# Kernel tuning notes

Hardware: AMD Instinct MI355X
Metric: run time of the kernel (lower is better)

Reference implementation:

```python
import jax, jax.numpy as jnp
import numpy as np

NUM_HEADS = 8
HEAD_DIM = 32  # in_channels // num_heads = 256 // 8


def setup_inputs() -> dict:
    key = jax.random.key(0)
    k1, k2, k3, k4 = jax.random.split(key, 4)
    B, C, H, W = 16, 256, 64, 64
    N = (H // 2) * (W // 2)  # 1024
    return {
        "x": jax.random.normal(k1, (B, C, H, W), dtype=jnp.float32),
        "w_qkv": jax.random.normal(k2, (3 * C, C), dtype=jnp.float32) * (1.0 / np.sqrt(C)),
        "b_qkv": jax.random.normal(k3, (3 * C,), dtype=jnp.float32) * 0.02,
        "pos_encoding": jax.random.normal(k4, (1, N, HEAD_DIM), dtype=jnp.float32) * 0.02,
    }


def reference(x, w_qkv, b_qkv, pos_encoding):
    B, C, H, W = x.shape
    Hp, Wp = H // 2, W // 2
    N = Hp * Wp
    # 1x1 conv: [B,C,H,W] -> [B,3C,H,W]
    y = jnp.einsum('bchw,oc->bohw', x, w_qkv) + b_qkv[None, :, None, None]
    # 2x2 max pool, stride 2
    y = y.reshape(B, 3 * C, Hp, 2, Wp, 2).max(axis=(3, 5))  # [B,3C,Hp,Wp]
    # split into q,k,v heads: channel order is (3, heads, head_dim)
    qkv = y.reshape(B, 3, NUM_HEADS, HEAD_DIM, N)
    qkv = qkv.transpose(1, 0, 2, 4, 3)  # [3,B,h,N,d]
    q, k, v = qkv[0], qkv[1], qkv[2]
    q = q + pos_encoding[:, None, :, :]  # broadcast over heads -> [B,h,N,d]
    scale = HEAD_DIM ** (-0.5)
    attn = jnp.einsum('bhnd,bhmd->bhnm', q, k) * scale
    attn = jax.nn.softmax(attn, axis=-1)
    out = jnp.einsum('bhnm,bhmd->bhnd', attn, v)  # [B,h,N,d]
    # transpose(2,3) then reshape -> [B, C, Hp, Wp]
    out = out.transpose(0, 1, 3, 2).reshape(B, C, Hp, Wp)
    return out
```

## Files before the change

### kernel.cpp

```cpp
#include <hip/hip_runtime.h>
#include <hip/hip_bf16.h>

typedef __bf16 bf16;
typedef bf16 bf16x8 __attribute__((ext_vector_type(8)));
typedef float f32x4 __attribute__((ext_vector_type(4)));
typedef float f32x16 __attribute__((ext_vector_type(16)));
typedef unsigned int u32;
typedef u32 u32x2 __attribute__((ext_vector_type(2)));
typedef u32 u32x4 __attribute__((ext_vector_type(4)));
typedef int i32x2 __attribute__((ext_vector_type(2)));


__device__ __forceinline__ u32 packbf2(float lo, float hi) {
    unsigned short a = __builtin_bit_cast(unsigned short, (bf16)lo);
    unsigned short b = __builtin_bit_cast(unsigned short, (bf16)hi);
    return (u32)a | ((u32)b << 16);
}

#if __has_builtin(__builtin_amdgcn_exp2f)
#define EXP2(x) __builtin_amdgcn_exp2f(x)
#else
#define EXP2(x) __expf((x)*0.69314718055994531f)
#endif

__device__ __forceinline__ i32x2 pl32swap(u32 a, u32 b) {
#if __has_builtin(__builtin_amdgcn_permlane32_swap)
    return __builtin_amdgcn_permlane32_swap((int)a, (int)b, false, false);
#else
    int lid = __builtin_amdgcn_mbcnt_hi(~0u, __builtin_amdgcn_mbcnt_lo(~0u, 0));
    u32 ax = (u32)__shfl_xor((int)a, 32);
    u32 bx = (u32)__shfl_xor((int)b, 32);
    i32x2 r;
    r.x = (int)(lid < 32 ? a : bx);
    r.y = (int)(lid < 32 ? ax : b);
    return r;
#endif
}

__device__ __forceinline__ f32x16 zero16() {
    f32x16 z;
#pragma unroll
    for (int i = 0; i < 16; ++i) z[i] = 0.f;
    return z;
}

__device__ __forceinline__ void gload_lds16(const bf16* gsrc, bf16* ldst) {
    __builtin_amdgcn_global_load_lds(
        (const __attribute__((address_space(1))) void*)gsrc,
        (__attribute__((address_space(3))) void*)ldst, 16, 0, 0);
}

#define MEMFENCE()                               \
    do {                                         \
        asm volatile("" ::: "memory");           \
        __builtin_amdgcn_sched_barrier(0);       \
    } while (0)

#define WAITV(N)                                                   \
    do {                                                           \
        asm volatile("s_waitcnt vmcnt(" #N ")" ::: "memory");      \
        __builtin_amdgcn_sched_barrier(0);                         \
    } while (0)

#define WAITLGKM()                                                 \
    do {                                                           \
        asm volatile("s_waitcnt lgkmcnt(0)" ::: "memory");         \
        __builtin_amdgcn_sched_barrier(0);                         \
    } while (0)

__global__ __launch_bounds__(256) void k_transpose_x(const float* __restrict__ x,
                                                     bf16* __restrict__ xt) {
    __shared__ __align__(16) bf16 tile[64][72];
    int b = blockIdx.z, cb = blockIdx.y, pb = blockIdx.x;
    int c0 = cb * 64, p0 = pb * 64;
    int t = threadIdx.x;
    int pr = (t & 15) * 4;
    int cr = t >> 4;
    const float* xp = x + ((size_t)(b * 256 + c0)) * 4096 + p0;
    for (int pass = 0; pass < 4; ++pass) {
        int c = cr + pass * 16;
        float4 v = *reinterpret_cast<const float4*>(xp + (size_t)c * 4096 + pr);
        tile[pr + 0][c] = (bf16)v.x;
        tile[pr + 1][c] = (bf16)v.y;
        tile[pr + 2][c] = (bf16)v.z;
        tile[pr + 3][c] = (bf16)v.w;
    }
    __syncthreads();
    bf16* op = xt + ((size_t)(b * 4096 + p0)) * 256 + c0;
    int c8 = (t & 7) * 8;
    int prow = t >> 3;
    for (int pass = 0; pass < 2; ++pass) {
        int p = prow + pass * 32;
        *reinterpret_cast<bf16x8*>(op + (size_t)p * 256 + c8) =
            *reinterpret_cast<const bf16x8*>(&tile[p][c8]);
    }
}

__global__ __launch_bounds__(256) void k_convert_w(const float* __restrict__ w,
                                                   bf16* __restrict__ wb) {
    int i = (blockIdx.x * 256 + threadIdx.x) * 8;
    float4 a = *reinterpret_cast<const float4*>(w + i);
    float4 b4 = *reinterpret_cast<const float4*>(w + i + 4);
    bf16x8 o;
    o[0] = (bf16)a.x;  o[1] = (bf16)a.y;  o[2] = (bf16)a.z;  o[3] = (bf16)a.w;
    o[4] = (bf16)b4.x; o[5] = (bf16)b4.y; o[6] = (bf16)b4.z; o[7] = (bf16)b4.w;
    *reinterpret_cast<bf16x8*>(wb + i) = o;
}

__global__ __launch_bounds__(256) void k_gemm_pool(const bf16* __restrict__ xt,
                                                   const bf16* __restrict__ wb,
                                                   const float* __restrict__ bias,
                                                   const float* __restrict__ pos,
                                                   bf16* __restrict__ Qb,
                                                   bf16* __restrict__ Kb,
                                                   bf16* __restrict__ Vb) {
    __shared__ __align__(16) bf16 bt[128 * 256];
    int b = blockIdx.y, nt = blockIdx.x;
    int p0 = nt * 128;
    int t = threadIdx.x;
    int w = t >> 6, lane = t & 63, g = lane >> 4, q = lane & 15;

    const bf16* xtp = xt + ((size_t)(b * 4096 + p0)) * 256;
    const bf16* wb_w = wb + (size_t)(w * 32) * 256;

    {
        int srow = t >> 5;
        int scb = t & 31;
        int wbase_row = w * 2;
#pragma unroll
        for (int pass = 0; pass < 16; ++pass) {
            int row = srow + pass * 8;
            int p = 2 * (row & 15) + ((row >> 4) & 1) + ((row >> 5) & 1) * 64 +
                    ((row >> 6) & 1) * 32;
            const bf16* gs = xtp + (size_t)p * 256 + ((scb ^ (row & 7)) << 3);
            gload_lds16(gs, bt + (pass * 8 + wbase_row) * 256);
        }
    }
    MEMFENCE();

    bf16x8 Ac[4], An[4];
#define LOADA(MT, KC, DST)                                                     \
    {                                                                          \
        _Pragma("unroll")                                                      \
        for (int ks = 0; ks < 2; ++ks)                                         \
            _Pragma("unroll")                                                  \
            for (int fr = 0; fr < 2; ++fr)                                     \
                DST[ks * 2 + fr] = *reinterpret_cast<const bf16x8*>(           \
                    wb_w + (size_t)((MT) * 128 + fr * 16 + q) * 256 +          \
                    (KC) * 64 + ks * 32 + g * 8);                              \
    }
    LOADA(0, 0, Ac);
    MEMFENCE();

    WAITV(4);
    __builtin_amdgcn_s_barrier();
    __builtin_amdgcn_sched_barrier(0);

    const float QSCALE = 0.2550406682649681f;

    for (int mt = 0; mt < 6; ++mt) {
        f32x4 acc[2][8];
#pragma unroll
        for (int fr = 0; fr < 2; ++fr)
#pragma unroll
            for (int fc = 0; fc < 8; ++fc) acc[fr][fc] = (f32x4){0.f, 0.f, 0.f, 0.f};

#pragma unroll
        for (int kc = 0; kc < 4; ++kc) {
            if (kc < 3) {
                LOADA(mt, kc + 1, An);
            } else if (mt < 5) {
                LOADA(mt + 1, 0, An);
            }
#pragma unroll
            for (int ks = 0; ks < 2; ++ks) {
#pragma unroll
                for (int fc = 0; fc < 8; ++fc) {
                    int co = kc * 64 + (((ks * 4 + g) ^ (q & 7)) << 3);
                    bf16x8 bfv = *reinterpret_cast<const bf16x8*>(
                        &bt[(fc * 16 + q) * 256 + co]);
                    acc[0][fc] = __builtin_amdgcn_mfma_f32_16x16x32_bf16(
                        Ac[ks * 2 + 0], bfv, acc[0][fc], 0, 0, 0);
                    acc[1][fc] = __builtin_amdgcn_mfma_f32_16x16x32_bf16(
                        Ac[ks * 2 + 1], bfv, acc[1][fc], 0, 0, 0);
                }
            }
#pragma unroll
            for (int i = 0; i < 4; ++i) Ac[i] = An[i];
        }

        int m0 = mt * 128;
        int sec = mt >> 1;
        int hh = ((m0 >> 5) + w) & 7;
        size_t bh = (size_t)(b * 8 + hh) * 32768;
#pragma unroll
        for (int fr = 0; fr < 2; ++fr) {
            int dbase = fr * 16 + g * 4;
            float4 bs = *reinterpret_cast<const float4*>(&bias[m0 + w * 32 + dbase]);
#pragma unroll
            for (int G = 0; G < 2; ++G) {
                int n_g = nt * 32 + G * 16 + q;
                float vm[4];
#pragma unroll
                for (int r = 0; r < 4; ++r) {
                    float a0 = fmaxf(acc[fr][4 * G + 0][r], acc[fr][4 * G + 1][r]);
                    float a1 = fmaxf(acc[fr][4 * G + 2][r], acc[fr][4 * G + 3][r]);
                    vm[r] = fmaxf(a0, a1) + ((const float*)&bs)[r];
                }
                if (sec == 0) {
                    float4 pv = *reinterpret_cast<const float4*>(
                        &pos[(size_t)n_g * 32 + dbase]);
                    u32x2 o2 = {packbf2((vm[0] + pv.x) * QSCALE, (vm[1] + pv.y) * QSCALE),
                                packbf2((vm[2] + pv.z) * QSCALE, (vm[3] + pv.w) * QSCALE)};
                    *reinterpret_cast<u32x2*>(Qb + bh + (size_t)n_g * 32 + dbase) = o2;
                } else if (sec == 1) {
                    u32x2 o2 = {packbf2(vm[0], vm[1]), packbf2(vm[2], vm[3])};
                    *reinterpret_cast<u32x2*>(Kb + bh + (size_t)n_g * 32 + dbase) = o2;
                } else {
#pragma unroll
                    for (int r = 0; r < 4; ++r)
                        Vb[bh + (size_t)(dbase + r) * 1024 + n_g] = (bf16)vm[r];
                }
            }
        }
    }
#undef LOADA
}

__global__ __launch_bounds__(256) void k_attn(const bf16* __restrict__ Q,
                                              const bf16* __restrict__ K,
                                              const bf16* __restrict__ V,
                                              float* __restrict__ out) {
    __shared__ __align__(16) bf16 kt[2][1024];
    __shared__ __align__(16) bf16 vt[2][1024];
    int h = blockIdx.x, b = blockIdx.y, qb = blockIdx.z;
    int t = threadIdx.x, w = t >> 6, lane = t & 63;
    int lq = lane & 31, hi = lane >> 5, hi8 = hi * 8;
    size_t bh = (size_t)b * 8 + h;
    const bf16* Qp = Q + bh * 32768;
    const bf16* Kp = K + bh * 32768;
    const bf16* Vp = V + bh * 32768;
    float* Op = out + ((size_t)(b * 256 + h * 32)) * 1024;
    int q0 = qb * 128 + w * 32;

    bf16x8 qf0 = *reinterpret_cast<const bf16x8*>(Qp + (size_t)(q0 + lq) * 32 + hi8);
    bf16x8 qf1 = *reinterpret_cast<const bf16x8*>(Qp + (size_t)(q0 + lq) * 32 + 16 + hi8);

    int sc = ((w & 1) << 1) + (lane >> 5);
    int srow = lane & 31;
    const bf16* sgK = Kp + (size_t)srow * 32 + sc * 8;
    const bf16* sgV = Vp + (size_t)srow * 1024 + sc * 8;
    int sdst = (w & 1) * 512;

#define STAGEKV(BB, KK)                                                        \
    do {                                                                       \
        int key0_ = (KK) * 32;                                                 \
        if (w < 2) gload_lds16(sgK + (size_t)key0_ * 32, &kt[BB][sdst]);       \
        else       gload_lds16(sgV + key0_, &vt[BB][sdst]);                    \
    } while (0)

    STAGEKV(0, 0);
    MEMFENCE();
    STAGEKV(1, 1);
    MEMFENCE();

    f32x16 o = zero16();
    float run_s = 0.f;

    for (int kk = 0; kk < 32; ++kk) {
        int cur = kk & 1;
        if (kk < 31) { WAITV(1); } else { WAITV(0); }
        __builtin_amdgcn_s_barrier();
        __builtin_amdgcn_sched_barrier(0);

        bf16x8 k0c = *reinterpret_cast<const bf16x8*>(&kt[cur][hi * 256 + lq * 8]);
        bf16x8 k1c = *reinterpret_cast<const bf16x8*>(&kt[cur][(2 + hi) * 256 + lq * 8]);
        bf16x8 v0c = *reinterpret_cast<const bf16x8*>(&vt[cur][hi * 256 + lq * 8]);
        bf16x8 v1c = *reinterpret_cast<const bf16x8*>(&vt[cur][(2 + hi) * 256 + lq * 8]);
        WAITLGKM();
        __builtin_amdgcn_s_barrier();
        __builtin_amdgcn_sched_barrier(0);
        if (kk < 30) STAGEKV(cur, kk + 2);
        MEMFENCE();

        f32x16 s = __builtin_amdgcn_mfma_f32_32x32x16_bf16(k0c, qf0, zero16(), 0, 0, 0);
        s = __builtin_amdgcn_mfma_f32_32x32x16_bf16(k1c, qf1, s, 0, 0, 0);

        float p[16];
#pragma unroll
        for (int r = 0; r < 16; ++r) p[r] = EXP2(s[r]);
        float ts = (((p[0] + p[1]) + (p[2] + p[3])) + ((p[4] + p[5]) + (p[6] + p[7]))) +
                   (((p[8] + p[9]) + (p[10] + p[11])) + ((p[12] + p[13]) + (p[14] + p[15])));
        run_s += ts;

        u32 pk0 = packbf2(p[0], p[1]),   pk1 = packbf2(p[2], p[3]);
        u32 pk2 = packbf2(p[4], p[5]),   pk3 = packbf2(p[6], p[7]);
        u32 pk4 = packbf2(p[8], p[9]),   pk5 = packbf2(p[10], p[11]);
        u32 pk6 = packbf2(p[12], p[13]), pk7 = packbf2(p[14], p[15]);

        i32x2 r02 = pl32swap(pk0, pk2);
        i32x2 r13 = pl32swap(pk1, pk3);
        i32x2 r46 = pl32swap(pk4, pk6);
        i32x2 r57 = pl32swap(pk5, pk7);

        u32x4 b0v = {(u32)r02.x, (u32)r13.x, (u32)r02.y, (u32)r13.y};
        u32x4 b1v = {(u32)r46.x, (u32)r57.x, (u32)r46.y, (u32)r57.y};
        bf16x8 pb0 = __builtin_bit_cast(bf16x8, b0v);
        bf16x8 pb1 = __builtin_bit_cast(bf16x8, b1v);

        o = __builtin_amdgcn_mfma_f32_32x32x16_bf16(v0c, pb0, o, 0, 0, 0);
        o = __builtin_amdgcn_mfma_f32_32x32x16_bf16(v1c, pb1, o, 0, 0, 0);
    }
#undef STAGEKV

    i32x2 rs = pl32swap(__builtin_bit_cast(u32, run_s), __builtin_bit_cast(u32, run_s));
    float tot = __builtin_bit_cast(float, (u32)rs.x) + __builtin_bit_cast(float, (u32)rs.y);
    float inv = 1.0f / tot;

#pragma unroll
    for (int r = 0; r < 16; ++r) {
        int dd = (r & 3) + 8 * (r >> 2) + 4 * hi;
        Op[(size_t)dd * 1024 + q0 + lq] = o[r] * inv;
    }
}

extern "C" void kernel_launch(void* const* d_in, const int* in_sizes, int n_in,
                              void* d_out, int out_size, void* d_ws, size_t ws_size,
                              hipStream_t stream) {
    const float* x = (const float*)d_in[0];
    const float* w = (const float*)d_in[1];
    const float* bias = (const float*)d_in[2];
    const float* pos = (const float*)d_in[3];
    float* outp = (float*)d_out;

    char* ws = (char*)d_ws;
    bf16* xt = (bf16*)(ws);
    bf16* wb = (bf16*)(ws + 33554432);
    bf16* Qb = (bf16*)(ws + 33947648);
    bf16* Kb = (bf16*)(ws + 42336256);
    bf16* Vb = (bf16*)(ws + 50724864);

    k_transpose_x<<<dim3(64, 4, 16), 256, 0, stream>>>(x, xt);
    k_convert_w<<<dim3(96), 256, 0, stream>>>(w, wb);
    k_gemm_pool<<<dim3(32, 16), 256, 0, stream>>>(xt, wb, bias, pos, Qb, Kb, Vb);
    k_attn<<<dim3(8, 16, 8), 256, 0, stream>>>(Qb, Kb, Vb, outp);
}
```

Measured before the change: 103.3 us.

## Split attention key range across wave pairs and combine partial sums in LDS

The attention block grows to 512 threads. Each pair of waves shares a 32-query tile and each wave handles half of the 1024 keys, which halves the serial loop from 32 to 16 iterations. Partial outputs and softmax denominators are merged through an LDS buffer before the final normalized store. This raises waves per block and per CU to hide latency, at the cost of more LDS, an extra block-wide barrier and a combine step. The combine is valid because the kernel uses no running max, only exp sums.

```diff
diff --git a/kernel.cpp b/kernel.cpp
--- a/kernel.cpp
+++ b/kernel.cpp
@@ -227,36 +227,41 @@
 #undef LOADA
 }
 
-__global__ __launch_bounds__(256) void k_attn(const bf16* __restrict__ Q,
-                                              const bf16* __restrict__ K,
-                                              const bf16* __restrict__ V,
-                                              float* __restrict__ out) {
-    __shared__ __align__(16) bf16 kt[2][1024];
-    __shared__ __align__(16) bf16 vt[2][1024];
+__global__ __launch_bounds__(512, 8) void k_attn(const bf16* __restrict__ Q,
+                                                 const bf16* __restrict__ K,
+                                                 const bf16* __restrict__ V,
+                                                 float* __restrict__ out) {
+    __shared__ __align__(16) bf16 kt[2][2][1024];
+    __shared__ __align__(16) bf16 vt[2][2][1024];
+    __shared__ float cmb[4][64][17];
     int h = blockIdx.x, b = blockIdx.y, qb = blockIdx.z;
     int t = threadIdx.x, w = t >> 6, lane = t & 63;
+    int pair = w >> 1, kh = w & 1;
     int lq = lane & 31, hi = lane >> 5, hi8 = hi * 8;
     size_t bh = (size_t)b * 8 + h;
     const bf16* Qp = Q + bh * 32768;
     const bf16* Kp = K + bh * 32768;
     const bf16* Vp = V + bh * 32768;
     float* Op = out + ((size_t)(b * 256 + h * 32)) * 1024;
-    int q0 = qb * 128 + w * 32;
+    int q0 = qb * 128 + pair * 32;
 
     bf16x8 qf0 = *reinterpret_cast<const bf16x8*>(Qp + (size_t)(q0 + lq) * 32 + hi8);
     bf16x8 qf1 = *reinterpret_cast<const bf16x8*>(Qp + (size_t)(q0 + lq) * 32 + 16 + hi8);
 
-    int sc = ((w & 1) << 1) + (lane >> 5);
+    int isV = w >> 2;
+    int tkh = (w >> 1) & 1;
+    int hf = w & 1;
+    int sc = (hf << 1) + (lane >> 5);
     int srow = lane & 31;
     const bf16* sgK = Kp + (size_t)srow * 32 + sc * 8;
     const bf16* sgV = Vp + (size_t)srow * 1024 + sc * 8;
-    int sdst = (w & 1) * 512;
+    int sdst = hf * 512;
 
 #define STAGEKV(BB, KK)                                                        \
     do {                                                                       \
-        int key0_ = (KK) * 32;                                                 \
-        if (w < 2) gload_lds16(sgK + (size_t)key0_ * 32, &kt[BB][sdst]);       \
-        else       gload_lds16(sgV + key0_, &vt[BB][sdst]);                    \
+        int key0_ = tkh * 512 + (KK) * 32;                                     \
+        if (!isV) gload_lds16(sgK + (size_t)key0_ * 32, &kt[BB][tkh][sdst]);   \
+        else      gload_lds16(sgV + key0_,              &vt[BB][tkh][sdst]);   \
     } while (0)
 
     STAGEKV(0, 0);
@@ -267,20 +272,20 @@
     f32x16 o = zero16();
     float run_s = 0.f;
 
-    for (int kk = 0; kk < 32; ++kk) {
+    for (int kk = 0; kk < 16; ++kk) {
         int cur = kk & 1;
-        if (kk < 31) { WAITV(1); } else { WAITV(0); }
+        if (kk < 15) { WAITV(1); } else { WAITV(0); }
         __builtin_amdgcn_s_barrier();
         __builtin_amdgcn_sched_barrier(0);
 
-        bf16x8 k0c = *reinterpret_cast<const bf16x8*>(&kt[cur][hi * 256 + lq * 8]);
-        bf16x8 k1c = *reinterpret_cast<const bf16x8*>(&kt[cur][(2 + hi) * 256 + lq * 8]);
-        bf16x8 v0c = *reinterpret_cast<const bf16x8*>(&vt[cur][hi * 256 + lq * 8]);
-        bf16x8 v1c = *reinterpret_cast<const bf16x8*>(&vt[cur][(2 + hi) * 256 + lq * 8]);
+        bf16x8 k0c = *reinterpret_cast<const bf16x8*>(&kt[cur][kh][hi * 256 + lq * 8]);
+        bf16x8 k1c = *reinterpret_cast<const bf16x8*>(&kt[cur][kh][(2 + hi) * 256 + lq * 8]);
+        bf16x8 v0c = *reinterpret_cast<const bf16x8*>(&vt[cur][kh][hi * 256 + lq * 8]);
+        bf16x8 v1c = *reinterpret_cast<const bf16x8*>(&vt[cur][kh][(2 + hi) * 256 + lq * 8]);
         WAITLGKM();
         __builtin_amdgcn_s_barrier();
         __builtin_amdgcn_sched_barrier(0);
-        if (kk < 30) STAGEKV(cur, kk + 2);
+        if (kk < 14) STAGEKV(cur, kk + 2);
         MEMFENCE();
 
         f32x16 s = __builtin_amdgcn_mfma_f32_32x32x16_bf16(k0c, qf0, zero16(), 0, 0, 0);
@@ -313,14 +318,26 @@
     }
 #undef STAGEKV
 
-    i32x2 rs = pl32swap(__builtin_bit_cast(u32, run_s), __builtin_bit_cast(u32, run_s));
-    float tot = __builtin_bit_cast(float, (u32)rs.x) + __builtin_bit_cast(float, (u32)rs.y);
-    float inv = 1.0f / tot;
-
-#pragma unroll
-    for (int r = 0; r < 16; ++r) {
-        int dd = (r & 3) + 8 * (r >> 2) + 4 * hi;
-        Op[(size_t)dd * 1024 + q0 + lq] = o[r] * inv;
+    if (kh) {
+#pragma unroll
+        for (int r = 0; r < 16; ++r) cmb[pair][lane][r] = o[r];
+        cmb[pair][lane][16] = run_s;
+    }
+    __syncthreads();
+    if (!kh) {
+#pragma unroll
+        for (int r = 0; r < 16; ++r) o[r] += cmb[pair][lane][r];
+        run_s += cmb[pair][lane][16];
+
+        i32x2 rs = pl32swap(__builtin_bit_cast(u32, run_s), __builtin_bit_cast(u32, run_s));
+        float tot = __builtin_bit_cast(float, (u32)rs.x) + __builtin_bit_cast(float, (u32)rs.y);
+        float inv = 1.0f / tot;
+
+#pragma unroll
+        for (int r = 0; r < 16; ++r) {
+            int dd = (r & 3) + 8 * (r >> 2) + 4 * hi;
+            Op[(size_t)dd * 1024 + q0 + lq] = o[r] * inv;
+        }
     }
 }
 
@@ -343,5 +360,5 @@
     k_transpose_x<<<dim3(64, 4, 16), 256, 0, stream>>>(x, xt);
     k_convert_w<<<dim3(96), 256, 0, stream>>>(w, wb);
     k_gemm_pool<<<dim3(32, 16), 256, 0, stream>>>(xt, wb, bias, pos, Qb, Kb, Vb);
-    k_attn<<<dim3(8, 16, 8), 256, 0, stream>>>(Qb, Kb, Vb, outp);
-}
+    k_attn<<<dim3(8, 16, 8), 512, 0, stream>>>(Qb, Kb, Vb, outp);
+}
```

After: 101.2 us. 1.02x faster.

## Process two query tiles per wave and stage 64 keys per iteration

Applied to the files above, without the earlier changes.

Each wave in the attention kernel now holds two 32-row query tiles, so every K/V fragment loaded from LDS feeds twice as many MFMAs. The stage size grows to 64 keys per loop trip, which halves the number of barrier/wait rounds, and the grid shrinks to half the query blocks. The aim is to cut LDS and global K/V traffic per unit of work and reduce synchronisation overhead. In exchange it raises register pressure from the two accumulators and two score tiles, and the fewer, larger blocks may lower occupancy or leave some CUs idle.

```diff
diff --git a/kernel.cpp b/kernel.cpp
--- a/kernel.cpp
+++ b/kernel.cpp
@@ -227,12 +227,57 @@
 #undef LOADA
 }
 
+#define SUB2(K0, K1, V0, V1)                                                   \
+    {                                                                          \
+        f32x16 sa = __builtin_amdgcn_mfma_f32_32x32x16_bf16(K0, qfa0, zero16(), 0, 0, 0); \
+        sa = __builtin_amdgcn_mfma_f32_32x32x16_bf16(K1, qfa1, sa, 0, 0, 0);   \
+        f32x16 sb = __builtin_amdgcn_mfma_f32_32x32x16_bf16(K0, qfb0, zero16(), 0, 0, 0); \
+        sb = __builtin_amdgcn_mfma_f32_32x32x16_bf16(K1, qfb1, sb, 0, 0, 0);   \
+        float pa[16], pb[16];                                                  \
+        _Pragma("unroll")                                                      \
+        for (int r = 0; r < 16; ++r) pa[r] = EXP2(sa[r]);                      \
+        _Pragma("unroll")                                                      \
+        for (int r = 0; r < 16; ++r) pb[r] = EXP2(sb[r]);                      \
+        run_a += (((pa[0]+pa[1])+(pa[2]+pa[3]))+((pa[4]+pa[5])+(pa[6]+pa[7]))) + \
+                 (((pa[8]+pa[9])+(pa[10]+pa[11]))+((pa[12]+pa[13])+(pa[14]+pa[15]))); \
+        run_b += (((pb[0]+pb[1])+(pb[2]+pb[3]))+((pb[4]+pb[5])+(pb[6]+pb[7]))) + \
+                 (((pb[8]+pb[9])+(pb[10]+pb[11]))+((pb[12]+pb[13])+(pb[14]+pb[15]))); \
+        {                                                                      \
+            u32 k0 = packbf2(pa[0],pa[1]),   k1 = packbf2(pa[2],pa[3]);        \
+            u32 k2 = packbf2(pa[4],pa[5]),   k3 = packbf2(pa[6],pa[7]);        \
+            u32 k4 = packbf2(pa[8],pa[9]),   k5 = packbf2(pa[10],pa[11]);      \
+            u32 k6 = packbf2(pa[12],pa[13]), k7 = packbf2(pa[14],pa[15]);      \
+            i32x2 r02 = pl32swap(k0, k2); i32x2 r13 = pl32swap(k1, k3);        \
+            i32x2 r46 = pl32swap(k4, k6); i32x2 r57 = pl32swap(k5, k7);        \
+            u32x4 b0v = {(u32)r02.x, (u32)r13.x, (u32)r02.y, (u32)r13.y};      \
+            u32x4 b1v = {(u32)r46.x, (u32)r57.x, (u32)r46.y, (u32)r57.y};      \
+            bf16x8 pb0 = __builtin_bit_cast(bf16x8, b0v);                      \
+            bf16x8 pb1 = __builtin_bit_cast(bf16x8, b1v);                      \
+            oa = __builtin_amdgcn_mfma_f32_32x32x16_bf16(V0, pb0, oa, 0, 0, 0);\
+            oa = __builtin_amdgcn_mfma_f32_32x32x16_bf16(V1, pb1, oa, 0, 0, 0);\
+        }                                                                      \
+        {                                                                      \
+            u32 k0 = packbf2(pb[0],pb[1]),   k1 = packbf2(pb[2],pb[3]);        \
+            u32 k2 = packbf2(pb[4],pb[5]),   k3 = packbf2(pb[6],pb[7]);        \
+            u32 k4 = packbf2(pb[8],pb[9]),   k5 = packbf2(pb[10],pb[11]);      \
+            u32 k6 = packbf2(pb[12],pb[13]), k7 = packbf2(pb[14],pb[15]);      \
+            i32x2 r02 = pl32swap(k0, k2); i32x2 r13 = pl32swap(k1, k3);        \
+            i32x2 r46 = pl32swap(k4, k6); i32x2 r57 = pl32swap(k5, k7);        \
+            u32x4 b0v = {(u32)r02.x, (u32)r13.x, (u32)r02.y, (u32)r13.y};      \
+            u32x4 b1v = {(u32)r46.x, (u32)r57.x, (u32)r46.y, (u32)r57.y};      \
+            bf16x8 pb0 = __builtin_bit_cast(bf16x8, b0v);                      \
+            bf16x8 pb1 = __builtin_bit_cast(bf16x8, b1v);                      \
+            ob = __builtin_amdgcn_mfma_f32_32x32x16_bf16(V0, pb0, ob, 0, 0, 0);\
+            ob = __builtin_amdgcn_mfma_f32_32x32x16_bf16(V1, pb1, ob, 0, 0, 0);\
+        }                                                                      \
+    }
+
 __global__ __launch_bounds__(256) void k_attn(const bf16* __restrict__ Q,
                                               const bf16* __restrict__ K,
                                               const bf16* __restrict__ V,
                                               float* __restrict__ out) {
-    __shared__ __align__(16) bf16 kt[2][1024];
-    __shared__ __align__(16) bf16 vt[2][1024];
+    __shared__ __align__(16) bf16 kt[2][2048];
+    __shared__ __align__(16) bf16 vt[2][2048];
     int h = blockIdx.x, b = blockIdx.y, qb = blockIdx.z;
     int t = threadIdx.x, w = t >> 6, lane = t & 63;
     int lq = lane & 31, hi = lane >> 5, hi8 = hi * 8;
@@ -241,86 +286,77 @@
     const bf16* Kp = K + bh * 32768;
     const bf16* Vp = V + bh * 32768;
     float* Op = out + ((size_t)(b * 256 + h * 32)) * 1024;
-    int q0 = qb * 128 + w * 32;
-
-    bf16x8 qf0 = *reinterpret_cast<const bf16x8*>(Qp + (size_t)(q0 + lq) * 32 + hi8);
-    bf16x8 qf1 = *reinterpret_cast<const bf16x8*>(Qp + (size_t)(q0 + lq) * 32 + 16 + hi8);
-
-    int sc = ((w & 1) << 1) + (lane >> 5);
+    int q0 = qb * 256 + w * 32;
+
+    bf16x8 qfa0 = *reinterpret_cast<const bf16x8*>(Qp + (size_t)(q0 + lq) * 32 + hi8);
+    bf16x8 qfa1 = *reinterpret_cast<const bf16x8*>(Qp + (size_t)(q0 + lq) * 32 + 16 + hi8);
+    bf16x8 qfb0 = *reinterpret_cast<const bf16x8*>(Qp + (size_t)(q0 + 128 + lq) * 32 + hi8);
+    bf16x8 qfb1 = *reinterpret_cast<const bf16x8*>(Qp + (size_t)(q0 + 128 + lq) * 32 + 16 + hi8);
+
     int srow = lane & 31;
-    const bf16* sgK = Kp + (size_t)srow * 32 + sc * 8;
-    const bf16* sgV = Vp + (size_t)srow * 1024 + sc * 8;
-    int sdst = (w & 1) * 512;
-
-#define STAGEKV(BB, KK)                                                        \
+    int sh = w & 1, isV = w >> 1;
+    const bf16* sg0;
+    if (!isV) sg0 = Kp + (size_t)(sh * 32 + srow) * 32 + (lane >> 5) * 8;
+    else      sg0 = Vp + (size_t)srow * 1024 + sh * 32 + (lane >> 5) * 8;
+    const bf16* sg1 = sg0 + 16;
+    int d0 = sh * 1024, d1 = sh * 1024 + 512;
+
+#define STAGE64(BB, TT)                                                        \
     do {                                                                       \
-        int key0_ = (KK) * 32;                                                 \
-        if (w < 2) gload_lds16(sgK + (size_t)key0_ * 32, &kt[BB][sdst]);       \
-        else       gload_lds16(sgV + key0_, &vt[BB][sdst]);                    \
+        if (!isV) {                                                            \
+            gload_lds16(sg0 + (size_t)(TT) * 2048, &kt[BB][d0]);               \
+            gload_lds16(sg1 + (size_t)(TT) * 2048, &kt[BB][d1]);               \
+        } else {                                                               \
+            gload_lds16(sg0 + (TT) * 64, &vt[BB][d0]);                         \
+            gload_lds16(sg1 + (TT) * 64, &vt[BB][d1]);                         \
+        }                                                                      \
     } while (0)
 
-    STAGEKV(0, 0);
+    f32x16 oa = zero16(), ob = zero16();
+    float run_a = 0.f, run_b = 0.f;
+
+    STAGE64(0, 0);
     MEMFENCE();
-    STAGEKV(1, 1);
+    STAGE64(1, 1);
     MEMFENCE();
 
-    f32x16 o = zero16();
-    float run_s = 0.f;
-
-    for (int kk = 0; kk < 32; ++kk) {
-        int cur = kk & 1;
-        if (kk < 31) { WAITV(1); } else { WAITV(0); }
+    for (int tt = 0; tt < 16; ++tt) {
+        int cur = tt & 1;
+        if (tt < 15) { WAITV(2); } else { WAITV(0); }
         __builtin_amdgcn_s_barrier();
         __builtin_amdgcn_sched_barrier(0);
 
-        bf16x8 k0c = *reinterpret_cast<const bf16x8*>(&kt[cur][hi * 256 + lq * 8]);
-        bf16x8 k1c = *reinterpret_cast<const bf16x8*>(&kt[cur][(2 + hi) * 256 + lq * 8]);
-        bf16x8 v0c = *reinterpret_cast<const bf16x8*>(&vt[cur][hi * 256 + lq * 8]);
-        bf16x8 v1c = *reinterpret_cast<const bf16x8*>(&vt[cur][(2 + hi) * 256 + lq * 8]);
+        bf16x8 ka0 = *reinterpret_cast<const bf16x8*>(&kt[cur][hi * 256 + lq * 8]);
+        bf16x8 ka1 = *reinterpret_cast<const bf16x8*>(&kt[cur][512 + hi * 256 + lq * 8]);
+        bf16x8 va0 = *reinterpret_cast<const bf16x8*>(&vt[cur][hi * 256 + lq * 8]);
+        bf16x8 va1 = *reinterpret_cast<const bf16x8*>(&vt[cur][512 + hi * 256 + lq * 8]);
+        bf16x8 kb0 = *reinterpret_cast<const bf16x8*>(&kt[cur][1024 + hi * 256 + lq * 8]);
+        bf16x8 kb1 = *reinterpret_cast<const bf16x8*>(&kt[cur][1536 + hi * 256 + lq * 8]);
+        bf16x8 vb0 = *reinterpret_cast<const bf16x8*>(&vt[cur][1024 + hi * 256 + lq * 8]);
+        bf16x8 vb1 = *reinterpret_cast<const bf16x8*>(&vt[cur][1536 + hi * 256 + lq * 8]);
         WAITLGKM();
         __builtin_amdgcn_s_barrier();
         __builtin_amdgcn_sched_barrier(0);
-        if (kk < 30) STAGEKV(cur, kk + 2);
+        if (tt < 14) STAGE64(cur, tt + 2);
         MEMFENCE();
 
-        f32x16 s = __builtin_amdgcn_mfma_f32_32x32x16_bf16(k0c, qf0, zero16(), 0, 0, 0);
-        s = __builtin_amdgcn_mfma_f32_32x32x16_bf16(k1c, qf1, s, 0, 0, 0);
-
-        float p[16];
-#pragma unroll
-        for (int r = 0; r < 16; ++r) p[r] = EXP2(s[r]);
-        float ts = (((p[0] + p[1]) + (p[2] + p[3])) + ((p[4] + p[5]) + (p[6] + p[7]))) +
-                   (((p[8] + p[9]) + (p[10] + p[11])) + ((p[12] + p[13]) + (p[14] + p[15])));
-        run_s += ts;
-
-        u32 pk0 = packbf2(p[0], p[1]),   pk1 = packbf2(p[2], p[3]);
-        u32 pk2 = packbf2(p[4], p[5]),   pk3 = packbf2(p[6], p[7]);
-        u32 pk4 = packbf2(p[8], p[9]),   pk5 = packbf2(p[10], p[11]);
-        u32 pk6 = packbf2(p[12], p[13]), pk7 = packbf2(p[14], p[15]);
-
-        i32x2 r02 = pl32swap(pk0, pk2);
-        i32x2 r13 = pl32swap(pk1, pk3);
-        i32x2 r46 = pl32swap(pk4, pk6);
-        i32x2 r57 = pl32swap(pk5, pk7);
-
-        u32x4 b0v = {(u32)r02.x, (u32)r13.x, (u32)r02.y, (u32)r13.y};
-        u32x4 b1v = {(u32)r46.x, (u32)r57.x, (u32)r46.y, (u32)r57.y};
-        bf16x8 pb0 = __builtin_bit_cast(bf16x8, b0v);
-        bf16x8 pb1 = __builtin_bit_cast(bf16x8, b1v);
-
-        o = __builtin_amdgcn_mfma_f32_32x32x16_bf16(v0c, pb0, o, 0, 0, 0);
-        o = __builtin_amdgcn_mfma_f32_32x32x16_bf16(v1c, pb1, o, 0, 0, 0);
-    }
-#undef STAGEKV
-
-    i32x2 rs = pl32swap(__builtin_bit_cast(u32, run_s), __builtin_bit_cast(u32, run_s));
-    float tot = __builtin_bit_cast(float, (u32)rs.x) + __builtin_bit_cast(float, (u32)rs.y);
-    float inv = 1.0f / tot;
+        SUB2(ka0, ka1, va0, va1);
+        SUB2(kb0, kb1, vb0, vb1);
+    }
+#undef STAGE64
+
+    i32x2 rsa = pl32swap(__builtin_bit_cast(u32, run_a), __builtin_bit_cast(u32, run_a));
+    float inva = 1.0f / (__builtin_bit_cast(float, (u32)rsa.x) +
+                         __builtin_bit_cast(float, (u32)rsa.y));
+    i32x2 rsb = pl32swap(__builtin_bit_cast(u32, run_b), __builtin_bit_cast(u32, run_b));
+    float invb = 1.0f / (__builtin_bit_cast(float, (u32)rsb.x) +
+                         __builtin_bit_cast(float, (u32)rsb.y));
 
 #pragma unroll
     for (int r = 0; r < 16; ++r) {
         int dd = (r & 3) + 8 * (r >> 2) + 4 * hi;
-        Op[(size_t)dd * 1024 + q0 + lq] = o[r] * inv;
+        Op[(size_t)dd * 1024 + q0 + lq] = oa[r] * inva;
+        Op[(size_t)dd * 1024 + q0 + 128 + lq] = ob[r] * invb;
     }
 }
 
@@ -343,5 +379,5 @@
     k_transpose_x<<<dim3(64, 4, 16), 256, 0, stream>>>(x, xt);
     k_convert_w<<<dim3(96), 256, 0, stream>>>(w, wb);
     k_gemm_pool<<<dim3(32, 16), 256, 0, stream>>>(xt, wb, bias, pos, Qb, Kb, Vb);
-    k_attn<<<dim3(8, 16, 8), 256, 0, stream>>>(Qb, Kb, Vb, outp);
-}
+    k_attn<<<dim3(8, 16, 4), 256, 0, stream>>>(Qb, Kb, Vb, outp);
+}
```

Measured after the change: 99.51 us. 1.04x faster.
